# Performance work log

Hardware: AMD Instinct MI355X
Metric: run time of the kernel (lower is better)

Reference implementation:

```python
import jax, jax.numpy as jnp
import numpy as np

SEQ, B, OBS, H = 128, 256, 64, 1024

def setup_inputs() -> dict:
    key = jax.random.key(0)
    ks = jax.random.split(key, 16)
    s = 0.03  # keep weights small so tanh/sigmoid stay in a sane range
    n = lambda k, shape, sc=s: jax.random.normal(k, shape, jnp.float32) * sc
    return {
        "x": jax.random.normal(ks[0], (SEQ * B, OBS), jnp.float32),
        "done": jax.random.randint(ks[1], (SEQ * B,), 0, 2).astype(jnp.int32),
        "h0": n(ks[2], (2, B, H), 0.1),
        "c0": n(ks[3], (2, B, H), 0.1),
        "W_ih0": n(ks[4], (4 * H, OBS)),
        "W_hh0": n(ks[5], (4 * H, H)),
        "b_ih0": jnp.zeros((4 * H,), jnp.float32),
        "b_hh0": jnp.zeros((4 * H,), jnp.float32),
        "W_ih1": n(ks[6], (4 * H, H)),
        "W_hh1": n(ks[7], (4 * H, H)),
        "b_ih1": jnp.zeros((4 * H,), jnp.float32),
        "b_hh1": jnp.zeros((4 * H,), jnp.float32),
        "ln_g": jnp.ones((H,), jnp.float32),
        "ln_b": jnp.zeros((H,), jnp.float32),
        "W1": n(ks[8], (512, H)),
        "b1": jnp.zeros((512,), jnp.float32),
        "W2": n(ks[9], (128, 512)),
        "b2": jnp.zeros((128,), jnp.float32),
        "W3": n(ks[10], (64, 128)),
        "b3": jnp.zeros((64,), jnp.float32),
        "Wv": n(ks[11], (1, 64)),
        "bv": jnp.zeros((1,), jnp.float32),
    }

def _lstm_cell(xin, h, c, Wih, Whh, bih, bhh):
    # PyTorch gate order: input, forget, cell(g), output
    g = xin @ Wih.T + bih + h @ Whh.T + bhh
    i, f, gg, o = jnp.split(g, 4, axis=-1)
    c2 = jax.nn.sigmoid(f) * c + jax.nn.sigmoid(i) * jnp.tanh(gg)
    h2 = jax.nn.sigmoid(o) * jnp.tanh(c2)
    return h2, c2

def reference(x, done, h0, c0, W_ih0, W_hh0, b_ih0, b_hh0, W_ih1, W_hh1,
              b_ih1, b_hh1, ln_g, ln_b, W1, b1, W2, b2, W3, b3, Wv, bv):
    batch = h0.shape[1]
    obs = x.shape[-1]
    xs = x.reshape(-1, batch, obs)                      # (S, B, obs)
    ds = done.reshape(-1, batch).astype(x.dtype)        # (S, B)

    def step(carry, td):
        h, c = carry                                    # each (2, B, H)
        xt, dt = td
        m = (1.0 - dt)[:, None]                         # reset mask (B, 1)
        h0_, c0_ = _lstm_cell(xt, h[0] * m, c[0] * m, W_ih0, W_hh0, b_ih0, b_hh0)
        h1_, c1_ = _lstm_cell(h0_, h[1] * m, c[1] * m, W_ih1, W_hh1, b_ih1, b_hh1)
        return (jnp.stack([h0_, h1_]), jnp.stack([c0_, c1_])), h1_

    (hN, cN), hs = jax.lax.scan(step, (h0, c0), (xs, ds))
    hidden = hs.reshape(-1, hs.shape[-1])               # (S*B, H)

    # LayerNorm (eps = 1e-5, torch default)
    mu = hidden.mean(-1, keepdims=True)
    var = jnp.mean(jnp.square(hidden - mu), -1, keepdims=True)
    hn = (hidden - mu) * jax.lax.rsqrt(var + 1e-5) * ln_g + ln_b

    a = jax.nn.elu(hn @ W1.T + b1)
    a = jax.nn.elu(a @ W2.T + b2)
    a = jax.nn.elu(a @ W3.T + b3)
    value = a @ Wv.T + bv                               # (S*B, 1)
    return value, hN, cN
```

## Files before the change

kernel.cpp:

```cpp
#include <hip/hip_runtime.h>
#include <cstdint>
#include <cstddef>

typedef unsigned short u16;
typedef __attribute__((ext_vector_type(8))) short short8;
typedef __attribute__((ext_vector_type(4))) float f32x4;

#define SEQ 128
#define BATCH 256
#define HID 1024
#define LSZ 262144

#define MFMA(a,b,c) __builtin_amdgcn_mfma_f32_16x16x32_bf16((a),(b),(c),0,0,0)

#define GLDS_CG(g, l) __builtin_amdgcn_global_load_lds( \
  (__attribute__((address_space(1))) void*)(uintptr_t)(const void*)(g), \
  (__attribute__((address_space(3))) void*)(unsigned)(uintptr_t)(void*)(l), 16, 0, 17)
#define GLDS_NC(g, l) __builtin_amdgcn_global_load_lds( \
  (__attribute__((address_space(1))) void*)(uintptr_t)(const void*)(g), \
  (__attribute__((address_space(3))) void*)(unsigned)(uintptr_t)(void*)(l), 16, 0, 0)

__device__ __forceinline__ u16 f2b(float f) {
  union { float f; unsigned u; } v; v.f = f;
  unsigned r = (v.u + 0x7FFFu + ((v.u >> 16) & 1u)) >> 16;
  return (u16)r;
}
__device__ __forceinline__ float b2f(u16 h) {
  union { unsigned u; float f; } v; v.u = ((unsigned)h) << 16; return v.f;
}
__device__ __forceinline__ float sigm(float x){ return 1.f/(1.f + __expf(-x)); }
__device__ __forceinline__ float tanh_f(float x){
  x = fminf(15.f, fmaxf(-15.f, x));
  float e = __expf(2.f*x); return (e-1.f)/(e+1.f);
}
__device__ __forceinline__ float eluf(float x){ return x > 0.f ? x : expm1f(x); }

__device__ __forceinline__ void store_cg(u16* p, short8 v) {
  asm volatile("global_store_dwordx4 %0, %1, off sc0 sc1" :: "v"(p), "v"(v) : "memory");
}
__device__ __forceinline__ void wait_vm0() {
  asm volatile("s_waitcnt vmcnt(0)" ::: "memory");
}
__device__ __forceinline__ void waitgroup(int* f, int tgt) {
  if (threadIdx.x < 64) {
    int idx = threadIdx.x & 31;
    while (__hip_atomic_load(f + idx, __ATOMIC_RELAXED, __HIP_MEMORY_SCOPE_AGENT) < tgt)
      __builtin_amdgcn_s_sleep(1);
  }
  asm volatile("" ::: "memory");
  __builtin_amdgcn_s_barrier();
  __builtin_amdgcn_sched_barrier(0);
}
__device__ __forceinline__ void waitgroup2(int* fa, int ta, int* fb, int tb) {
  if (threadIdx.x < 64) {
    int idx = threadIdx.x & 31;
    int* p  = (threadIdx.x < 32) ? (fa + idx) : (fb + idx);
    int tgt = (threadIdx.x < 32) ? ta : tb;
    while (__hip_atomic_load(p, __ATOMIC_RELAXED, __HIP_MEMORY_SCOPE_AGENT) < tgt)
      __builtin_amdgcn_s_sleep(1);
  }
  asm volatile("" ::: "memory");
  __builtin_amdgcn_s_barrier();
  __builtin_amdgcn_sched_barrier(0);
}

static const size_t OFF_W0F  = 0;
static const size_t OFF_W1F  = 8912896;
static const size_t OFF_XF   = 25690112;
static const size_t OFF_C0   = 30932992;
static const size_t OFF_C1   = 31981568;
static const size_t OFF_H1U  = 33030144;
static const size_t OFF_BS0  = 100663296;
static const size_t OFF_BS1  = 100679680;
static const size_t OFF_MU   = 100697088;
static const size_t OFF_RSTD = 100828160;
static const size_t OFF_W1LN = 100959232;
static const size_t OFF_S1   = 102007808;
static const size_t OFF_B1P  = 102009856;
static const size_t OFF_W2B  = 102011904;
static const size_t OFF_W3B  = 102142976;
static const size_t OFF_A1   = 102159360;
static const size_t OFF_A2   = 0;
static const size_t OFF_A3   = 8912896;
static const size_t OFF_H0M  = 102159360;
static const size_t OFF_H1M  = 102159360 + 1048576;
static const size_t OFF_H0U  = 102159360 + 2097152;

__global__ void prep_wf(const float* __restrict__ wih, const float* __restrict__ whh,
                        u16* __restrict__ out, int nkb, int kx) {
  int b = blockIdx.x; int cg = b >> 3, ct = b & 7;
  int g = ct >> 1;
  int n = nkb << 9;
  for (int e = threadIdx.x; e < n; e += 256) {
    int kb = e >> 9, r = e & 511;
    int q = r >> 7, col16 = (r >> 3) & 15, j = r & 7;
    int hl = (ct & 1) * 16 + col16;
    int gr = g * HID + cg * 32 + hl;
    int k = kb * 32 + q * 8 + j;
    float w = (k < kx) ? wih[(size_t)gr * kx + k] : whh[(size_t)gr * HID + (k - kx)];
    out[((size_t)(cg * nkb + kb) * 8 + ct) * 512 + r] = f2b(w);
  }
}

__global__ void prep_w1ln(const float* __restrict__ w1, const float* __restrict__ lng,
                          const float* __restrict__ lnb, const float* __restrict__ b1,
                          u16* __restrict__ w1ln, float* __restrict__ S1, float* __restrict__ b1p) {
  int j = blockIdx.x;
  float s = 0.f, bb = 0.f;
  for (int k = threadIdx.x; k < HID; k += 256) {
    float w = w1[(size_t)j * HID + k];
    u16 q = f2b(w * lng[k]);
    w1ln[(size_t)j * HID + k] = q;
    s += b2f(q);
    bb += w * lnb[k];
  }
  __shared__ float r1[256], r2[256];
  r1[threadIdx.x] = s; r2[threadIdx.x] = bb;
  __syncthreads();
  for (int o = 128; o > 0; o >>= 1) {
    if (threadIdx.x < (unsigned)o) { r1[threadIdx.x] += r1[threadIdx.x+o]; r2[threadIdx.x] += r2[threadIdx.x+o]; }
    __syncthreads();
  }
  if (threadIdx.x == 0) { S1[j] = r1[0]; b1p[j] = b1[j] + r2[0]; }
}

__global__ void prep_misc(const float* bih0, const float* bhh0, const float* bih1, const float* bhh1,
                          const float* x, const float* h0in, const float* c0in,
                          const float* w2, const float* w3, const int* done,
                          float* bs0, float* bs1, u16* xf, u16* h0m, u16* h1m,
                          float* c0buf, float* c1buf, u16* w2b, u16* w3b, int* flg) {
  size_t i = (size_t)blockIdx.x * blockDim.x + threadIdx.x;
  if (i < 4096) { bs0[i] = bih0[i] + bhh0[i]; return; }
  i -= 4096;
  if (i < 4096) { bs1[i] = bih1[i] + bhh1[i]; return; }
  i -= 4096;
  if (i < 2097152) {
    int o = (int)i;
    int r = o & 511, tile = o >> 9;
    int q = r >> 7, rl = (r >> 3) & 15, j = r & 7;
    int kb = tile & 1, v = tile >> 1;
    int grt = v & 15, t = v >> 4;
    int row = grt * 16 + rl, k = kb * 32 + q * 8 + j;
    xf[o] = f2b(x[((size_t)t * BATCH + row) * 64 + k]);
    return;
  }
  i -= 2097152;
  if (i < 262144) {
    int o = (int)i;
    int r = o & 511, tile = o >> 9;
    int q = r >> 7, rl = (r >> 3) & 15, j = r & 7;
    int grt = tile >> 5, kb = tile & 31;
    int row = grt * 16 + rl, h = kb * 32 + q * 8 + j;
    h0m[o] = done[row] ? (u16)0 : f2b(h0in[(size_t)row * HID + h]);
    return;
  }
  i -= 262144;
  if (i < 262144) {
    int o = (int)i;
    int r = o & 511, tile = o >> 9;
    int q = r >> 7, rl = (r >> 3) & 15, j = r & 7;
    int grt = tile >> 5, kb = tile & 31;
    int row = grt * 16 + rl, h = kb * 32 + q * 8 + j;
    h1m[o] = done[row] ? (u16)0 : f2b(h0in[LSZ + (size_t)row * HID + h]);
    return;
  }
  i -= 262144;
  if (i < LSZ) { c0buf[i] = c0in[i]; return; }
  i -= LSZ;
  if (i < LSZ) { c1buf[i] = c0in[LSZ + i]; return; }
  i -= LSZ;
  if (i < 65536) { w2b[i] = f2b(w2[i]); return; }
  i -= 65536;
  if (i < 8192) { w3b[i] = f2b(w3[i]); return; }
  i -= 8192;
  if (i < 512) { flg[i] = 0; return; }
}

__global__ __launch_bounds__(256, 2) void lstm_persist(
    const u16* __restrict__ w0f, const u16* __restrict__ w1f, const u16* __restrict__ xf,
    u16* __restrict__ h0u, u16* __restrict__ h1u,
    u16* __restrict__ h0m, u16* __restrict__ h1m,
    float* __restrict__ c0b, float* __restrict__ c1b,
    const float* __restrict__ bs0, const float* __restrict__ bs1,
    const int* __restrict__ done, int* __restrict__ flg,
    float* __restrict__ dout)
{
  const int bid = blockIdx.x;
  const int layer = bid >> 8;
  const int rg = (bid >> 5) & 7;
  const int cg = bid & 31;
  const int tid = threadIdx.x;
  const int lane = tid & 63, wv = tid >> 6;
  const int quad = lane >> 4, c16 = lane & 15;
  const int NKB = layer ? 64 : 34;
  const int NC  = layer ? 16 : 9;
  const u16* Wf = layer ? w1f : w0f;
  const float* bs = layer ? bs1 : bs0;
  float* cb = layer ? c1b : c0b;
  int* fl0 = flg;
  int* fl1 = flg + 256;
  int* myf = (layer ? fl1 : fl0) + rg * 32 + cg;
  int* g0 = fl0 + rg * 32;
  int* g1 = fl1 + rg * 32;

  __shared__ __align__(16) u16 smem[32768];
  float* gl = (float*)smem;

  const short8 z8 = {0,0,0,0,0,0,0,0};

  for (int t = 0; t < SEQ; ++t) {
    if (layer == 0) {
      if (t >= 1) waitgroup(g0, t);
    } else {
      if (t >= 1) waitgroup2(g0, t + 1, g1, t);
      else        waitgroup(g0, 1);
    }

    auto issueA = [&](int p) {
      int oc = p; if (oc > NC - 1) oc = NC - 1;
      int kb = oc * 4 + wv; if (kb > NKB - 1) kb = NKB - 1;
      u16* lb = &smem[((unsigned)(p & 7)) * 4096 + (unsigned)wv * 1024];
      if (layer == 0) {
        if (kb < 2) {
          #pragma unroll
          for (int j = 0; j < 2; ++j) {
            const u16* g = xf + ((size_t)((t * 16 + rg * 2 + j) * 2 + kb)) * 512 + lane * 8;
            GLDS_NC(g, lb + j * 512);
          }
        } else {
          #pragma unroll
          for (int j = 0; j < 2; ++j) {
            const u16* g = h0m + (size_t)(t & 1) * 262144
                               + (size_t)((rg * 2 + j) * 32 + (kb - 2)) * 512 + lane * 8;
            GLDS_CG(g, lb + j * 512);
          }
        }
      } else {
        if (kb < 32) {
          #pragma unroll
          for (int j = 0; j < 2; ++j) {
            const u16* g = h0u + (size_t)((t + 1) & 3) * 262144
                               + (size_t)((rg * 2 + j) * 32 + kb) * 512 + lane * 8;
            GLDS_CG(g, lb + j * 512);
          }
        } else {
          #pragma unroll
          for (int j = 0; j < 2; ++j) {
            const u16* g = h1m + (size_t)(t & 1) * 262144
                               + (size_t)((rg * 2 + j) * 32 + (kb - 32)) * 512 + lane * 8;
            GLDS_CG(g, lb + j * 512);
          }
        }
      }
    };

    auto loadB = [&](int p, short8 (&vB)[4][2]) {
      int oc = p; if (oc > NC - 1) oc = NC - 1;
      #pragma unroll
      for (int kbl = 0; kbl < 4; ++kbl) {
        int kb = oc * 4 + kbl; if (kb > NKB - 1) kb = NKB - 1;
        #pragma unroll
        for (int h = 0; h < 2; ++h)
          vB[kbl][h] = *(const short8*)(Wf + ((size_t)(cg * NKB + kb) * 8 + wv * 2 + h) * 512 + lane * 8);
      }
    };

    f32x4 acc[2][2];
    #pragma unroll
    for (int a = 0; a < 2; ++a) { acc[a][0] = (f32x4){0,0,0,0}; acc[a][1] = (f32x4){0,0,0,0}; }

    auto comp = [&](int p, short8 (&vB)[4][2]) {
      int kbc = NKB - p * 4; if (kbc > 4) kbc = 4;
      const u16* sb = &smem[((unsigned)(p & 7)) * 4096] + lane * 8;
      #pragma unroll
      for (int kbl = 0; kbl < 4; ++kbl) if (kbl < kbc) {
        #pragma unroll
        for (int a = 0; a < 2; ++a) {
          short8 af = *(const short8*)(sb + (kbl * 2 + a) * 512);
          acc[a][0] = MFMA(af, vB[kbl][0], acc[a][0]);
          acc[a][1] = MFMA(af, vB[kbl][1], acc[a][1]);
        }
      }
    };

    short8 vB0[4][2], vB1[4][2], vB2[4][2], vB3[4][2];

    loadB(0, vB0);
    asm volatile("" ::: "memory");
    issueA(0);
    asm volatile("" ::: "memory");
    loadB(1, vB1);
    asm volatile("" ::: "memory");
    issueA(1);
    asm volatile("" ::: "memory");
    loadB(2, vB2);
    asm volatile("" ::: "memory");
    issueA(2);

#define CHUNK(CC, VBL, VBU) \
    loadB((CC) + 3, VBL); \
    asm volatile("" ::: "memory"); \
    issueA((CC) + 3); \
    asm volatile("s_waitcnt vmcnt(30)" ::: "memory"); \
    __builtin_amdgcn_s_barrier(); \
    __builtin_amdgcn_sched_barrier(0); \
    comp((CC), VBU);

    int c = 0;
    for (;;) {
      CHUNK(c, vB3, vB0) if (++c == NC) break;
      CHUNK(c, vB0, vB1) if (++c == NC) break;
      CHUNK(c, vB1, vB2) if (++c == NC) break;
      CHUNK(c, vB2, vB3) if (++c == NC) break;
    }
#undef CHUNK

    wait_vm0();
    __syncthreads();

    #pragma unroll
    for (int a = 0; a < 2; ++a)
      #pragma unroll
      for (int ct = 0; ct < 2; ++ct)
        #pragma unroll
        for (int rgi = 0; rgi < 4; ++rgi)
          gl[(a * 16 + quad * 4 + rgi) * 132 + wv * 32 + ct * 16 + c16] = acc[a][ct][rgi];
    __syncthreads();

    if (layer == 0 && t >= 4) waitgroup(g1, t - 3);

    if (tid < 128) {
      int row = tid >> 2;
      int q = tid & 3;
      int h8 = q * 8;
      int rowg = rg * 32 + row;
      int H0 = cg * 32 + h8;
      const float* glp = gl + row * 132;
      float m = done[t * BATCH + rowg] ? 0.f : 1.f;
      int nx = (t < SEQ - 1) ? done[(t + 1) * BATCH + rowg] : 0;
      float* cp = cb + (size_t)rowg * HID + H0;
      short8 hv;
      float h2a[8], c2a[8];
      #pragma unroll
      for (int j = 0; j < 8; ++j) {
        float ivv = glp[h8 + j]      + bs[H0 + j];
        float fvv = glp[32 + h8 + j] + bs[HID + H0 + j];
        float gvv = glp[64 + h8 + j] + bs[2*HID + H0 + j];
        float ovv = glp[96 + h8 + j] + bs[3*HID + H0 + j];
        float c2 = sigm(fvv) * (cp[j] * m) + sigm(ivv) * tanh_f(gvv);
        float h2 = sigm(ovv) * tanh_f(c2);
        cp[j] = c2;
        h2a[j] = h2; c2a[j] = c2;
        ((u16*)&hv)[j] = f2b(h2);
      }
      short8 hm = nx ? z8 : hv;
      size_t off = (size_t)((rg * 2 + (row >> 4)) * 32 + cg) * 512 + (size_t)(q * 16 + (row & 15)) * 8;
      if (layer == 0) {
        store_cg(h0u + (size_t)((t + 1) & 3) * 262144 + off, hv);
        if (t < SEQ - 1) store_cg(h0m + (size_t)((t + 1) & 1) * 262144 + off, hm);
      } else {
        store_cg(h1u + (size_t)(t + 1) * 262144 + off, hv);
        if (t < SEQ - 1) store_cg(h1m + (size_t)((t + 1) & 1) * 262144 + off, hm);
      }
      if (t == SEQ - 1) {
        float* dh = dout + 32768 + (size_t)layer * LSZ + (size_t)rowg * HID + H0;
        float* dc = dout + 32768 + 2 * LSZ + (size_t)layer * LSZ + (size_t)rowg * HID + H0;
        #pragma unroll
        for (int j = 0; j < 8; ++j) { dh[j] = h2a[j]; dc[j] = c2a[j]; }
      }
    }
    wait_vm0();
    __syncthreads();
    if (tid == 0) __hip_atomic_fetch_add(myf, 1, __ATOMIC_RELAXED, __HIP_MEMORY_SCOPE_AGENT);
  }
}

__global__ void ln_stats(const u16* __restrict__ h1u, float* __restrict__ mu, float* __restrict__ rstd) {
  int R = blockIdx.x * 4 + (threadIdx.x >> 6);
  int l = threadIdx.x & 63;
  int t = R >> 8, brow = R & 255, grt = brow >> 4, rl = brow & 15;
  const u16* base = h1u + (size_t)(t + 1) * 262144 + (size_t)(grt * 32 + (l >> 1)) * 512;
  int q2 = (l & 1) * 2;
  short8 v0 = *(const short8*)(base + (q2 * 16 + rl) * 8);
  short8 v1 = *(const short8*)(base + ((q2 + 1) * 16 + rl) * 8);
  float s = 0.f, q = 0.f;
  #pragma unroll
  for (int e = 0; e < 8; ++e) {
    float a = b2f((u16)v0[e]); s += a; q += a*a;
    float b = b2f((u16)v1[e]); s += b; q += b*b;
  }
  for (int o = 32; o > 0; o >>= 1) { s += __shfl_xor(s, o); q += __shfl_xor(q, o); }
  if (l == 0) {
    float mm = s * (1.f/1024.f);
    float var = q * (1.f/1024.f) - mm*mm;
    mu[R] = mm; rstd[R] = rsqrtf(var + 1e-5f);
  }
}

__global__ __launch_bounds__(512, 4) void mlp_gemm(
    const u16* __restrict__ A, int lda, int amode,
    const u16* __restrict__ B, int K, int N,
    u16* __restrict__ out, int ldo, int mode, int swiz,
    const float* __restrict__ mu, const float* __restrict__ rstd,
    const float* __restrict__ S1v, const float* __restrict__ bias)
{
  int nt, mtb;
  if (swiz) { int p = blockIdx.x * gridDim.y + blockIdx.y; nt = p & 3; mtb = p >> 2; }
  else { nt = blockIdx.x; mtb = blockIdx.y; }
  const int tid = threadIdx.x, lane = tid & 63, wv = tid >> 6;
  const int quad = lane >> 4, c16 = lane & 15;
  __shared__ __align__(16) u16 Am[16384], Bm[16384];
  f32x4 acc[8];
  #pragma unroll
  for (int i = 0; i < 8; ++i) acc[i] = (f32x4){0.f,0.f,0.f,0.f};

  int arow[4], akl[4], bcol[4];
  #pragma unroll
  for (int i = 0; i < 4; ++i) {
    int s = tid + i * 512, sub = s >> 6, lp = s & 63;
    int ks = sub >> 3, u = sub & 7;
    arow[i] = mtb * 128 + u * 16 + (lp & 15);
    akl[i]  = ks * 32 + (lp >> 4) * 8;
    bcol[i] = nt * 128 + u * 16 + (lp & 15);
  }
  short8 vA[4], vB[4];
  const short8 z8 = {0,0,0,0,0,0,0,0};
  const int NCH = K >> 7;
  auto load_stage = [&](int ci) {
    int kc = ci << 7;
    #pragma unroll
    for (int i = 0; i < 4; ++i) {
      if (amode) {
        int R = arow[i], k = kc + akl[i];
        const u16* p = A + (size_t)((R >> 8) + 1) * 262144
                         + (size_t)(((R >> 4) & 15) * 32 + (k >> 5)) * 512
                         + (size_t)((((k >> 3) & 3) * 16 + (R & 15)) * 8);
        vA[i] = *(const short8*)p;
      } else {
        vA[i] = *(const short8*)(A + (size_t)arow[i] * lda + kc + akl[i]);
      }
      vB[i] = (bcol[i] < N) ? *(const short8*)(B + (size_t)bcol[i] * K + kc + akl[i]) : z8;
    }
  };
  load_stage(0);
  for (int ci = 0; ci < NCH; ++ci) {
    #pragma unroll
    for (int i = 0; i < 4; ++i) {
      *(short8*)&Am[(size_t)(tid + i*512) * 8] = vA[i];
      *(short8*)&Bm[(size_t)(tid + i*512) * 8] = vB[i];
    }
    __syncthreads();
    if (ci + 1 < NCH) load_stage(ci + 1);
    #pragma unroll
    for (int ks = 0; ks < 4; ++ks) {
      short8 bf = *(const short8*)&Bm[((ks*8 + wv)*64 + lane) * 8];
      #pragma unroll
      for (int rt = 0; rt < 8; ++rt) {
        short8 af = *(const short8*)&Am[((ks*8 + rt)*64 + lane) * 8];
        acc[rt] = MFMA(af, bf, acc[rt]);
      }
    }
    __syncthreads();
  }
  int col = nt * 128 + wv * 16 + c16;
  if (col < N) {
    #pragma unroll
    for (int rt = 0; rt < 8; ++rt) {
      #pragma unroll
      for (int rgi = 0; rgi < 4; ++rgi) {
        int row = mtb * 128 + rt * 16 + quad * 4 + rgi;
        float v = acc[rt][rgi];
        if (mode == 0) v = v * rstd[row] - mu[row] * rstd[row] * S1v[col] + bias[col];
        else           v = v + bias[col];
        v = eluf(v);
        out[(size_t)row * ldo + col] = f2b(v);
      }
    }
  }
}

__global__ void value_head(const u16* __restrict__ a3, const float* __restrict__ wv,
                           const float* __restrict__ bv, float* __restrict__ dout) {
  int row = blockIdx.x * 256 + threadIdx.x;
  const short8* p = (const short8*)(a3 + (size_t)row * 64);
  float s = bv[0];
  #pragma unroll
  for (int j = 0; j < 8; ++j) {
    short8 v = p[j];
    #pragma unroll
    for (int e = 0; e < 8; ++e) s += b2f((u16)v[e]) * wv[j*8+e];
  }
  dout[row] = s;
}

extern "C" void kernel_launch(void* const* d_in, const int* in_sizes, int n_in,
                              void* d_out, int out_size, void* d_ws, size_t ws_size,
                              hipStream_t stream) {
  (void)in_sizes; (void)n_in; (void)out_size; (void)ws_size;
  const float* x    = (const float*)d_in[0];
  const int*   done = (const int*)d_in[1];
  const float* h0in = (const float*)d_in[2];
  const float* c0in = (const float*)d_in[3];
  const float* wih0 = (const float*)d_in[4];
  const float* whh0 = (const float*)d_in[5];
  const float* bih0 = (const float*)d_in[6];
  const float* bhh0 = (const float*)d_in[7];
  const float* wih1 = (const float*)d_in[8];
  const float* whh1 = (const float*)d_in[9];
  const float* bih1 = (const float*)d_in[10];
  const float* bhh1 = (const float*)d_in[11];
  const float* lng  = (const float*)d_in[12];
  const float* lnb  = (const float*)d_in[13];
  const float* w1   = (const float*)d_in[14];
  const float* b1   = (const float*)d_in[15];
  const float* w2   = (const float*)d_in[16];
  const float* b2   = (const float*)d_in[17];
  const float* w3   = (const float*)d_in[18];
  const float* b3   = (const float*)d_in[19];
  const float* wvp  = (const float*)d_in[20];
  const float* bvp  = (const float*)d_in[21];
  float* dout = (float*)d_out;
  char* ws = (char*)d_ws;

  u16*   w0f  = (u16*)(ws + OFF_W0F);
  u16*   w1f  = (u16*)(ws + OFF_W1F);
  u16*   xf   = (u16*)(ws + OFF_XF);
  u16*   h0u  = (u16*)(ws + OFF_H0U);
  u16*   h1u  = (u16*)(ws + OFF_H1U);
  u16*   h0m  = (u16*)(ws + OFF_H0M);
  u16*   h1m  = (u16*)(ws + OFF_H1M);
  float* c0b  = (float*)(ws + OFF_C0);
  float* c1b  = (float*)(ws + OFF_C1);
  float* bs0  = (float*)(ws + OFF_BS0);
  float* bs1  = (float*)(ws + OFF_BS1);
  int*   flg  = (int*)(ws + OFF_MU);
  float* mu   = (float*)(ws + OFF_MU);
  float* rstd = (float*)(ws + OFF_RSTD);
  u16*   w1ln = (u16*)(ws + OFF_W1LN);
  float* s1   = (float*)(ws + OFF_S1);
  float* b1p  = (float*)(ws + OFF_B1P);
  u16*   w2b  = (u16*)(ws + OFF_W2B);
  u16*   w3b  = (u16*)(ws + OFF_W3B);
  u16*   a1   = (u16*)(ws + OFF_A1);
  u16*   a2   = (u16*)(ws + OFF_A2);
  u16*   a3   = (u16*)(ws + OFF_A3);

  prep_wf<<<256, 256, 0, stream>>>(wih0, whh0, w0f, 34, 64);
  prep_wf<<<256, 256, 0, stream>>>(wih1, whh1, w1f, 64, 1024);
  prep_w1ln<<<512, 256, 0, stream>>>(w1, lng, lnb, b1, w1ln, s1, b1p);
  prep_misc<<<12610, 256, 0, stream>>>(bih0, bhh0, bih1, bhh1, x, h0in, c0in, w2, w3, done,
                                       bs0, bs1, xf, h0m, h1m, c0b, c1b, w2b, w3b, flg);

  lstm_persist<<<512, 256, 0, stream>>>(w0f, w1f, xf, h0u, h1u, h0m, h1m, c0b, c1b,
                                        bs0, bs1, done, flg, dout);

  ln_stats<<<8192, 256, 0, stream>>>(h1u, mu, rstd);
  mlp_gemm<<<dim3(8, 128), 512, 0, stream>>>(h1u, 0, 1, w1ln, 1024, 512, a1, 512, 0, 1, mu, rstd, s1, b1p);
  mlp_gemm<<<dim3(1, 256), 512, 0, stream>>>(a1, 512, 0, w2b, 512, 128, a2, 128, 1, 0, mu, rstd, s1, b2);
  mlp_gemm<<<dim3(1, 256), 512, 0, stream>>>(a2, 128, 0, w3b, 128, 64, a3, 64, 1, 0, mu, rstd, s1, b3);
  value_head<<<128, 256, 0, stream>>>(a3, wvp, bvp, dout);
}
```

Before: 2.778 ms.

## Use per-timestep hidden-state buffers to drop cross-layer wait and coherent loads

When the workspace is large enough, the h0u, h1m and h0m exchange buffers become per-timestep arrays instead of small ring buffers, chosen by a runtime tier from ws_size. Each slot is written only once, so readers can use non-temporal loads instead of system-coherent ones, and layer 0 no longer waits for layer 1 to free a ring slot. The intent is to cut inter-layer sync stalls and coherent-load cost. In exchange it uses far more workspace, and if ws_size is too small it falls back to the old ring path. Correctness relies on each slot being written exactly once per step.

New measurement: 3.395 ms. +22.2%, slower.

```diff
diff --git a/kernel.cpp b/kernel.cpp
--- a/kernel.cpp
+++ b/kernel.cpp
@@ -13,9 +13,12 @@
 
 #define MFMA(a,b,c) __builtin_amdgcn_mfma_f32_16x16x32_bf16((a),(b),(c),0,0,0)
 
-#define GLDS_CG(g, l) __builtin_amdgcn_global_load_lds( \
+#define GLDS_SC(g, l) __builtin_amdgcn_global_load_lds( \
   (__attribute__((address_space(1))) void*)(uintptr_t)(const void*)(g), \
   (__attribute__((address_space(3))) void*)(unsigned)(uintptr_t)(void*)(l), 16, 0, 17)
+#define GLDS_NT(g, l) __builtin_amdgcn_global_load_lds( \
+  (__attribute__((address_space(1))) void*)(uintptr_t)(const void*)(g), \
+  (__attribute__((address_space(3))) void*)(unsigned)(uintptr_t)(void*)(l), 16, 0, 2)
 #define GLDS_NC(g, l) __builtin_amdgcn_global_load_lds( \
   (__attribute__((address_space(1))) void*)(uintptr_t)(const void*)(g), \
   (__attribute__((address_space(3))) void*)(unsigned)(uintptr_t)(void*)(l), 16, 0, 0)
@@ -82,9 +85,15 @@
 static const size_t OFF_A1   = 102159360;
 static const size_t OFF_A2   = 0;
 static const size_t OFF_A3   = 8912896;
-static const size_t OFF_H0M  = 102159360;
-static const size_t OFF_H1M  = 102159360 + 1048576;
-static const size_t OFF_H0U  = 102159360 + 2097152;
+static const size_t OFF_H0M_R  = 102159360;
+static const size_t OFF_H1M_R  = 103207936;
+static const size_t OFF_H0U_R  = 104256512;
+static const size_t OFF_H0U_PT = 106353664;
+static const size_t OFF_H1M_PT = 173986816;
+static const size_t OFF_H0M_PT = 241095680;
+static const size_t NEED1 = 173986816;
+static const size_t NEED2 = 241095680;
+static const size_t NEED3 = 308204544;
 
 __global__ void prep_wf(const float* __restrict__ wih, const float* __restrict__ whh,
                         u16* __restrict__ out, int nkb, int kx) {
@@ -183,7 +192,7 @@
     float* __restrict__ c0b, float* __restrict__ c1b,
     const float* __restrict__ bs0, const float* __restrict__ bs1,
     const int* __restrict__ done, int* __restrict__ flg,
-    float* __restrict__ dout)
+    float* __restrict__ dout, int tier)
 {
   const int bid = blockIdx.x;
   const int layer = bid >> 8;
@@ -216,6 +225,10 @@
       else        waitgroup(g0, 1);
     }
 
+    const size_t s_h0m_r = (size_t)(tier >= 3 ? (unsigned)t : (unsigned)(t & 1)) * 262144;
+    const size_t s_h0u_r = (size_t)(tier >= 1 ? (unsigned)(t + 1) : (unsigned)((t + 1) & 3)) * 262144;
+    const size_t s_h1m_r = (size_t)(tier >= 2 ? (unsigned)t : (unsigned)(t & 1)) * 262144;
+
     auto issueA = [&](int p) {
       int oc = p; if (oc > NC - 1) oc = NC - 1;
       int kb = oc * 4 + wv; if (kb > NKB - 1) kb = NKB - 1;
@@ -230,25 +243,22 @@
         } else {
           #pragma unroll
           for (int j = 0; j < 2; ++j) {
-            const u16* g = h0m + (size_t)(t & 1) * 262144
-                               + (size_t)((rg * 2 + j) * 32 + (kb - 2)) * 512 + lane * 8;
-            GLDS_CG(g, lb + j * 512);
+            const u16* g = h0m + s_h0m_r + (size_t)((rg * 2 + j) * 32 + (kb - 2)) * 512 + lane * 8;
+            if (tier >= 3) { GLDS_NT(g, lb + j * 512); } else { GLDS_SC(g, lb + j * 512); }
           }
         }
       } else {
         if (kb < 32) {
           #pragma unroll
           for (int j = 0; j < 2; ++j) {
-            const u16* g = h0u + (size_t)((t + 1) & 3) * 262144
-                               + (size_t)((rg * 2 + j) * 32 + kb) * 512 + lane * 8;
-            GLDS_CG(g, lb + j * 512);
+            const u16* g = h0u + s_h0u_r + (size_t)((rg * 2 + j) * 32 + kb) * 512 + lane * 8;
+            if (tier >= 1) { GLDS_NT(g, lb + j * 512); } else { GLDS_SC(g, lb + j * 512); }
           }
         } else {
           #pragma unroll
           for (int j = 0; j < 2; ++j) {
-            const u16* g = h1m + (size_t)(t & 1) * 262144
-                               + (size_t)((rg * 2 + j) * 32 + (kb - 32)) * 512 + lane * 8;
-            GLDS_CG(g, lb + j * 512);
+            const u16* g = h1m + s_h1m_r + (size_t)((rg * 2 + j) * 32 + (kb - 32)) * 512 + lane * 8;
+            if (tier >= 2) { GLDS_NT(g, lb + j * 512); } else { GLDS_SC(g, lb + j * 512); }
           }
         }
       }
@@ -327,7 +337,7 @@
           gl[(a * 16 + quad * 4 + rgi) * 132 + wv * 32 + ct * 16 + c16] = acc[a][ct][rgi];
     __syncthreads();
 
-    if (layer == 0 && t >= 4) waitgroup(g1, t - 3);
+    if (layer == 0 && tier < 1 && t >= 4) waitgroup(g1, t - 3);
 
     if (tid < 128) {
       int row = tid >> 2;
@@ -355,12 +365,15 @@
       }
       short8 hm = nx ? z8 : hv;
       size_t off = (size_t)((rg * 2 + (row >> 4)) * 32 + cg) * 512 + (size_t)(q * 16 + (row & 15)) * 8;
+      size_t w_h0u = (size_t)(tier >= 1 ? (unsigned)(t + 1) : (unsigned)((t + 1) & 3)) * 262144;
+      size_t w_h0m = (size_t)(tier >= 3 ? (unsigned)(t + 1) : (unsigned)((t + 1) & 1)) * 262144;
+      size_t w_h1m = (size_t)(tier >= 2 ? (unsigned)(t + 1) : (unsigned)((t + 1) & 1)) * 262144;
       if (layer == 0) {
-        store_cg(h0u + (size_t)((t + 1) & 3) * 262144 + off, hv);
-        if (t < SEQ - 1) store_cg(h0m + (size_t)((t + 1) & 1) * 262144 + off, hm);
+        store_cg(h0u + w_h0u + off, hv);
+        if (t < SEQ - 1) store_cg(h0m + w_h0m + off, hm);
       } else {
         store_cg(h1u + (size_t)(t + 1) * 262144 + off, hv);
-        if (t < SEQ - 1) store_cg(h1m + (size_t)((t + 1) & 1) * 262144 + off, hm);
+        if (t < SEQ - 1) store_cg(h1m + w_h1m + off, hm);
       }
       if (t == SEQ - 1) {
         float* dh = dout + 32768 + (size_t)layer * LSZ + (size_t)rowg * HID + H0;
@@ -496,7 +509,7 @@
 extern "C" void kernel_launch(void* const* d_in, const int* in_sizes, int n_in,
                               void* d_out, int out_size, void* d_ws, size_t ws_size,
                               hipStream_t stream) {
-  (void)in_sizes; (void)n_in; (void)out_size; (void)ws_size;
+  (void)in_sizes; (void)n_in; (void)out_size;
   const float* x    = (const float*)d_in[0];
   const int*   done = (const int*)d_in[1];
   const float* h0in = (const float*)d_in[2];
@@ -522,13 +535,18 @@
   float* dout = (float*)d_out;
   char* ws = (char*)d_ws;
 
+  int tier = 0;
+  if (ws_size >= NEED3)      tier = 3;
+  else if (ws_size >= NEED2) tier = 2;
+  else if (ws_size >= NEED1) tier = 1;
+
   u16*   w0f  = (u16*)(ws + OFF_W0F);
   u16*   w1f  = (u16*)(ws + OFF_W1F);
   u16*   xf   = (u16*)(ws + OFF_XF);
-  u16*   h0u  = (u16*)(ws + OFF_H0U);
   u16*   h1u  = (u16*)(ws + OFF_H1U);
-  u16*   h0m  = (u16*)(ws + OFF_H0M);
-  u16*   h1m  = (u16*)(ws + OFF_H1M);
+  u16*   h0u  = (u16*)(ws + (tier >= 1 ? OFF_H0U_PT : OFF_H0U_R));
+  u16*   h1m  = (u16*)(ws + (tier >= 2 ? OFF_H1M_PT : OFF_H1M_R));
+  u16*   h0m  = (u16*)(ws + (tier >= 3 ? OFF_H0M_PT : OFF_H0M_R));
   float* c0b  = (float*)(ws + OFF_C0);
   float* c1b  = (float*)(ws + OFF_C1);
   float* bs0  = (float*)(ws + OFF_BS0);
@@ -552,7 +570,7 @@
                                        bs0, bs1, xf, h0m, h1m, c0b, c1b, w2b, w3b, flg);
 
   lstm_persist<<<512, 256, 0, stream>>>(w0f, w1f, xf, h0u, h1u, h0m, h1m, c0b, c1b,
-                                        bs0, bs1, done, flg, dout);
+                                        bs0, bs1, done, flg, dout, tier);
 
   ln_stats<<<8192, 256, 0, stream>>>(h1u, mu, rstd);
   mlp_gemm<<<dim3(8, 128), 512, 0, stream>>>(h1u, 0, 1, w1ln, 1024, 512, a1, 512, 0, 1, mu, rstd, s1, b1p);
```

## Load LSTM operands directly to registers and mask hidden state in-kernel

Applied to the files above, without the earlier changes.

Replaces the LDS staging pipeline (global_load_lds into an 8-deep shared ring with barriers) with direct register loads of A and B fragments, double-buffered over chunks of 2 k-blocks. The separate masked hidden-state buffers are dropped: the done mask is applied in registers with a bitwise AND at load time, so each step writes only one h store instead of two. The h0 history is now kept for all time steps instead of a 4-deep ring, which removes the cross-layer back-pressure wait. This trades LDS-based prefetch depth for fewer stores and barriers, at the risk of exposing global-load latency.

New measurement: 3.410 ms. +22.7%, slower.

```diff
diff --git a/kernel.cpp b/kernel.cpp
--- a/kernel.cpp
+++ b/kernel.cpp
@@ -5,6 +5,7 @@
 typedef unsigned short u16;
 typedef __attribute__((ext_vector_type(8))) short short8;
 typedef __attribute__((ext_vector_type(4))) float f32x4;
+typedef __attribute__((ext_vector_type(4))) unsigned uint4v;
 
 #define SEQ 128
 #define BATCH 256
@@ -13,13 +14,6 @@
 
 #define MFMA(a,b,c) __builtin_amdgcn_mfma_f32_16x16x32_bf16((a),(b),(c),0,0,0)
 
-#define GLDS_CG(g, l) __builtin_amdgcn_global_load_lds( \
-  (__attribute__((address_space(1))) void*)(uintptr_t)(const void*)(g), \
-  (__attribute__((address_space(3))) void*)(unsigned)(uintptr_t)(void*)(l), 16, 0, 17)
-#define GLDS_NC(g, l) __builtin_amdgcn_global_load_lds( \
-  (__attribute__((address_space(1))) void*)(uintptr_t)(const void*)(g), \
-  (__attribute__((address_space(3))) void*)(unsigned)(uintptr_t)(void*)(l), 16, 0, 0)
-
 __device__ __forceinline__ u16 f2b(float f) {
   union { float f; unsigned u; } v; v.f = f;
   unsigned r = (v.u + 0x7FFFu + ((v.u >> 16) & 1u)) >> 16;
@@ -34,6 +28,12 @@
   float e = __expf(2.f*x); return (e-1.f)/(e+1.f);
 }
 __device__ __forceinline__ float eluf(float x){ return x > 0.f ? x : expm1f(x); }
+
+__device__ __forceinline__ short8 andm(short8 v, unsigned m) {
+  uint4v u = __builtin_bit_cast(uint4v, v);
+  u &= m;
+  return __builtin_bit_cast(short8, u);
+}
 
 __device__ __forceinline__ void store_cg(u16* p, short8 v) {
   asm volatile("global_store_dwordx4 %0, %1, off sc0 sc1" :: "v"(p), "v"(v) : "memory");
@@ -82,9 +82,7 @@
 static const size_t OFF_A1   = 102159360;
 static const size_t OFF_A2   = 0;
 static const size_t OFF_A3   = 8912896;
-static const size_t OFF_H0M  = 102159360;
-static const size_t OFF_H1M  = 102159360 + 1048576;
-static const size_t OFF_H0U  = 102159360 + 2097152;
+static const size_t OFF_H0U  = 106353664;
 
 __global__ void prep_wf(const float* __restrict__ wih, const float* __restrict__ whh,
                         u16* __restrict__ out, int nkb, int kx) {
@@ -126,8 +124,8 @@
 
 __global__ void prep_misc(const float* bih0, const float* bhh0, const float* bih1, const float* bhh1,
                           const float* x, const float* h0in, const float* c0in,
-                          const float* w2, const float* w3, const int* done,
-                          float* bs0, float* bs1, u16* xf, u16* h0m, u16* h1m,
+                          const float* w2, const float* w3,
+                          float* bs0, float* bs1, u16* xf, u16* h0u, u16* h1u,
                           float* c0buf, float* c1buf, u16* w2b, u16* w3b, int* flg) {
   size_t i = (size_t)blockIdx.x * blockDim.x + threadIdx.x;
   if (i < 4096) { bs0[i] = bih0[i] + bhh0[i]; return; }
@@ -151,7 +149,7 @@
     int q = r >> 7, rl = (r >> 3) & 15, j = r & 7;
     int grt = tile >> 5, kb = tile & 31;
     int row = grt * 16 + rl, h = kb * 32 + q * 8 + j;
-    h0m[o] = done[row] ? (u16)0 : f2b(h0in[(size_t)row * HID + h]);
+    h0u[o] = f2b(h0in[(size_t)row * HID + h]);
     return;
   }
   i -= 262144;
@@ -161,7 +159,7 @@
     int q = r >> 7, rl = (r >> 3) & 15, j = r & 7;
     int grt = tile >> 5, kb = tile & 31;
     int row = grt * 16 + rl, h = kb * 32 + q * 8 + j;
-    h1m[o] = done[row] ? (u16)0 : f2b(h0in[LSZ + (size_t)row * HID + h]);
+    h1u[o] = f2b(h0in[LSZ + (size_t)row * HID + h]);
     return;
   }
   i -= 262144;
@@ -179,7 +177,6 @@
 __global__ __launch_bounds__(256, 2) void lstm_persist(
     const u16* __restrict__ w0f, const u16* __restrict__ w1f, const u16* __restrict__ xf,
     u16* __restrict__ h0u, u16* __restrict__ h1u,
-    u16* __restrict__ h0m, u16* __restrict__ h1m,
     float* __restrict__ c0b, float* __restrict__ c1b,
     const float* __restrict__ bs0, const float* __restrict__ bs1,
     const int* __restrict__ done, int* __restrict__ flg,
@@ -193,7 +190,7 @@
   const int lane = tid & 63, wv = tid >> 6;
   const int quad = lane >> 4, c16 = lane & 15;
   const int NKB = layer ? 64 : 34;
-  const int NC  = layer ? 16 : 9;
+  const int NC  = layer ? 32 : 17;
   const u16* Wf = layer ? w1f : w0f;
   const float* bs = layer ? bs1 : bs0;
   float* cb = layer ? c1b : c0b;
@@ -203,10 +200,7 @@
   int* g0 = fl0 + rg * 32;
   int* g1 = fl1 + rg * 32;
 
-  __shared__ __align__(16) u16 smem[32768];
-  float* gl = (float*)smem;
-
-  const short8 z8 = {0,0,0,0,0,0,0,0};
+  __shared__ __align__(16) float gl[32 * 132];
 
   for (int t = 0; t < SEQ; ++t) {
     if (layer == 0) {
@@ -216,118 +210,78 @@
       else        waitgroup(g0, 1);
     }
 
-    auto issueA = [&](int p) {
-      int oc = p; if (oc > NC - 1) oc = NC - 1;
-      int kb = oc * 4 + wv; if (kb > NKB - 1) kb = NKB - 1;
-      u16* lb = &smem[((unsigned)(p & 7)) * 4096 + (unsigned)wv * 1024];
-      if (layer == 0) {
-        if (kb < 2) {
-          #pragma unroll
-          for (int j = 0; j < 2; ++j) {
-            const u16* g = xf + ((size_t)((t * 16 + rg * 2 + j) * 2 + kb)) * 512 + lane * 8;
-            GLDS_NC(g, lb + j * 512);
-          }
-        } else {
-          #pragma unroll
-          for (int j = 0; j < 2; ++j) {
-            const u16* g = h0m + (size_t)(t & 1) * 262144
-                               + (size_t)((rg * 2 + j) * 32 + (kb - 2)) * 512 + lane * 8;
-            GLDS_CG(g, lb + j * 512);
-          }
-        }
-      } else {
-        if (kb < 32) {
-          #pragma unroll
-          for (int j = 0; j < 2; ++j) {
-            const u16* g = h0u + (size_t)((t + 1) & 3) * 262144
-                               + (size_t)((rg * 2 + j) * 32 + kb) * 512 + lane * 8;
-            GLDS_CG(g, lb + j * 512);
-          }
-        } else {
-          #pragma unroll
-          for (int j = 0; j < 2; ++j) {
-            const u16* g = h1m + (size_t)(t & 1) * 262144
-                               + (size_t)((rg * 2 + j) * 32 + (kb - 32)) * 512 + lane * 8;
-            GLDS_CG(g, lb + j * 512);
-          }
-        }
-      }
-    };
-
-    auto loadB = [&](int p, short8 (&vB)[4][2]) {
-      int oc = p; if (oc > NC - 1) oc = NC - 1;
-      #pragma unroll
-      for (int kbl = 0; kbl < 4; ++kbl) {
-        int kb = oc * 4 + kbl; if (kb > NKB - 1) kb = NKB - 1;
-        #pragma unroll
-        for (int h = 0; h < 2; ++h)
-          vB[kbl][h] = *(const short8*)(Wf + ((size_t)(cg * NKB + kb) * 8 + wv * 2 + h) * 512 + lane * 8);
-      }
-    };
+    unsigned msk[2];
+    #pragma unroll
+    for (int a = 0; a < 2; ++a) {
+      int row = rg * 32 + a * 16 + (lane & 15);
+      msk[a] = done[t * BATCH + row] ? 0u : 0xFFFFFFFFu;
+    }
+
+    const u16* a_x  = xf  + (size_t)(t * 16 + rg * 2) * 2 * 512 + lane * 8;
+    const u16* a_h0r = h0u + (size_t)t * 262144 + (size_t)(rg * 2) * 32 * 512 + lane * 8;
+    const u16* a_h0  = h0u + (size_t)(t + 1) * 262144 + (size_t)(rg * 2) * 32 * 512 + lane * 8;
+    const u16* a_h1  = h1u + (size_t)t * 262144 + (size_t)(rg * 2) * 32 * 512 + lane * 8;
+    const u16* b_w  = Wf + (size_t)(cg * NKB * 8 + wv * 2) * 512 + lane * 8;
 
     f32x4 acc[2][2];
     #pragma unroll
     for (int a = 0; a < 2; ++a) { acc[a][0] = (f32x4){0,0,0,0}; acc[a][1] = (f32x4){0,0,0,0}; }
 
-    auto comp = [&](int p, short8 (&vB)[4][2]) {
-      int kbc = NKB - p * 4; if (kbc > 4) kbc = 4;
-      const u16* sb = &smem[((unsigned)(p & 7)) * 4096] + lane * 8;
-      #pragma unroll
-      for (int kbl = 0; kbl < 4; ++kbl) if (kbl < kbc) {
-        #pragma unroll
-        for (int a = 0; a < 2; ++a) {
-          short8 af = *(const short8*)(sb + (kbl * 2 + a) * 512);
-          acc[a][0] = MFMA(af, vB[kbl][0], acc[a][0]);
-          acc[a][1] = MFMA(af, vB[kbl][1], acc[a][1]);
-        }
-      }
-    };
-
-    short8 vB0[4][2], vB1[4][2], vB2[4][2], vB3[4][2];
-
-    loadB(0, vB0);
-    asm volatile("" ::: "memory");
-    issueA(0);
-    asm volatile("" ::: "memory");
-    loadB(1, vB1);
-    asm volatile("" ::: "memory");
-    issueA(1);
-    asm volatile("" ::: "memory");
-    loadB(2, vB2);
-    asm volatile("" ::: "memory");
-    issueA(2);
-
-#define CHUNK(CC, VBL, VBU) \
-    loadB((CC) + 3, VBL); \
-    asm volatile("" ::: "memory"); \
-    issueA((CC) + 3); \
-    asm volatile("s_waitcnt vmcnt(30)" ::: "memory"); \
-    __builtin_amdgcn_s_barrier(); \
-    __builtin_amdgcn_sched_barrier(0); \
-    comp((CC), VBU);
-
+    short8 cA[2][2], cB[2][2], nA[2][2], nB[2][2];
+
+#define LOADC(CIN, AA, BB) { \
+    int cc = (CIN); if (cc > NC - 1) cc = NC - 1; \
+    _Pragma("unroll") for (int kbl = 0; kbl < 2; ++kbl) { \
+      int kb = cc * 2 + kbl; \
+      if (layer == 0) { \
+        if (kb < 2) { \
+          _Pragma("unroll") for (int a = 0; a < 2; ++a) \
+            AA[kbl][a] = *(const short8*)(a_x + (size_t)(a * 2 + kb) * 512); \
+        } else { \
+          _Pragma("unroll") for (int a = 0; a < 2; ++a) \
+            AA[kbl][a] = andm(*(const short8*)(a_h0r + (size_t)(a * 32 + (kb - 2)) * 512), msk[a]); \
+        } \
+      } else { \
+        if (kb < 32) { \
+          _Pragma("unroll") for (int a = 0; a < 2; ++a) \
+            AA[kbl][a] = *(const short8*)(a_h0 + (size_t)(a * 32 + kb) * 512); \
+        } else { \
+          _Pragma("unroll") for (int a = 0; a < 2; ++a) \
+            AA[kbl][a] = andm(*(const short8*)(a_h1 + (size_t)(a * 32 + (kb - 32)) * 512), msk[a]); \
+        } \
+      } \
+      _Pragma("unroll") for (int h = 0; h < 2; ++h) \
+        BB[kbl][h] = *(const short8*)(b_w + (size_t)(kb * 8 + h) * 512); \
+    } }
+
+#define COMPC(AA, BB) { \
+    _Pragma("unroll") for (int kbl = 0; kbl < 2; ++kbl) \
+      _Pragma("unroll") for (int a = 0; a < 2; ++a) { \
+        acc[a][0] = MFMA(AA[kbl][a], BB[kbl][0], acc[a][0]); \
+        acc[a][1] = MFMA(AA[kbl][a], BB[kbl][1], acc[a][1]); \
+      } }
+
+    LOADC(0, cA, cB)
     int c = 0;
     for (;;) {
-      CHUNK(c, vB3, vB0) if (++c == NC) break;
-      CHUNK(c, vB0, vB1) if (++c == NC) break;
-      CHUNK(c, vB1, vB2) if (++c == NC) break;
-      CHUNK(c, vB2, vB3) if (++c == NC) break;
-    }
-#undef CHUNK
-
-    wait_vm0();
-    __syncthreads();
+      LOADC(c + 1, nA, nB)
+      COMPC(cA, cB)
+      if (++c == NC) break;
+      LOADC(c + 1, cA, cB)
+      COMPC(nA, nB)
+      if (++c == NC) break;
+    }
+#undef LOADC
+#undef COMPC
 
     #pragma unroll
     for (int a = 0; a < 2; ++a)
       #pragma unroll
-      for (int ct = 0; ct < 2; ++ct)
+      for (int h = 0; h < 2; ++h)
         #pragma unroll
         for (int rgi = 0; rgi < 4; ++rgi)
-          gl[(a * 16 + quad * 4 + rgi) * 132 + wv * 32 + ct * 16 + c16] = acc[a][ct][rgi];
+          gl[(a * 16 + quad * 4 + rgi) * 132 + wv * 32 + h * 16 + c16] = acc[a][h][rgi];
     __syncthreads();
-
-    if (layer == 0 && t >= 4) waitgroup(g1, t - 3);
 
     if (tid < 128) {
       int row = tid >> 2;
@@ -337,7 +291,6 @@
       int H0 = cg * 32 + h8;
       const float* glp = gl + row * 132;
       float m = done[t * BATCH + rowg] ? 0.f : 1.f;
-      int nx = (t < SEQ - 1) ? done[(t + 1) * BATCH + rowg] : 0;
       float* cp = cb + (size_t)rowg * HID + H0;
       short8 hv;
       float h2a[8], c2a[8];
@@ -353,15 +306,9 @@
         h2a[j] = h2; c2a[j] = c2;
         ((u16*)&hv)[j] = f2b(h2);
       }
-      short8 hm = nx ? z8 : hv;
       size_t off = (size_t)((rg * 2 + (row >> 4)) * 32 + cg) * 512 + (size_t)(q * 16 + (row & 15)) * 8;
-      if (layer == 0) {
-        store_cg(h0u + (size_t)((t + 1) & 3) * 262144 + off, hv);
-        if (t < SEQ - 1) store_cg(h0m + (size_t)((t + 1) & 1) * 262144 + off, hm);
-      } else {
-        store_cg(h1u + (size_t)(t + 1) * 262144 + off, hv);
-        if (t < SEQ - 1) store_cg(h1m + (size_t)((t + 1) & 1) * 262144 + off, hm);
-      }
+      if (layer == 0) store_cg(h0u + (size_t)(t + 1) * 262144 + off, hv);
+      else            store_cg(h1u + (size_t)(t + 1) * 262144 + off, hv);
       if (t == SEQ - 1) {
         float* dh = dout + 32768 + (size_t)layer * LSZ + (size_t)rowg * HID + H0;
         float* dc = dout + 32768 + 2 * LSZ + (size_t)layer * LSZ + (size_t)rowg * HID + H0;
@@ -527,8 +474,6 @@
   u16*   xf   = (u16*)(ws + OFF_XF);
   u16*   h0u  = (u16*)(ws + OFF_H0U);
   u16*   h1u  = (u16*)(ws + OFF_H1U);
-  u16*   h0m  = (u16*)(ws + OFF_H0M);
-  u16*   h1m  = (u16*)(ws + OFF_H1M);
   float* c0b  = (float*)(ws + OFF_C0);
   float* c1b  = (float*)(ws + OFF_C1);
   float* bs0  = (float*)(ws + OFF_BS0);
@@ -548,10 +493,10 @@
   prep_wf<<<256, 256, 0, stream>>>(wih0, whh0, w0f, 34, 64);
   prep_wf<<<256, 256, 0, stream>>>(wih1, whh1, w1f, 64, 1024);
   prep_w1ln<<<512, 256, 0, stream>>>(w1, lng, lnb, b1, w1ln, s1, b1p);
-  prep_misc<<<12610, 256, 0, stream>>>(bih0, bhh0, bih1, bhh1, x, h0in, c0in, w2, w3, done,
-                                       bs0, bs1, xf, h0m, h1m, c0b, c1b, w2b, w3b, flg);
-
-  lstm_persist<<<512, 256, 0, stream>>>(w0f, w1f, xf, h0u, h1u, h0m, h1m, c0b, c1b,
+  prep_misc<<<12610, 256, 0, stream>>>(bih0, bhh0, bih1, bhh1, x, h0in, c0in, w2, w3,
+                                       bs0, bs1, xf, h0u, h1u, c0b, c1b, w2b, w3b, flg);
+
+  lstm_persist<<<512, 256, 0, stream>>>(w0f, w1f, xf, h0u, h1u, c0b, c1b,
                                         bs0, bs1, done, flg, dout);
 
   ln_stats<<<8192, 256, 0, stream>>>(h1u, mu, rstd);
```
